# Kernel tuning notes

Hardware: AMD Instinct MI355X
Metric: run time of the kernel (lower is better)

Reference implementation:

```python
import jax, jax.numpy as jnp
import numpy as np

EPS = 1e-5

def group_norm(x, gamma, beta):
    # GroupNorm(1, C) on [N, C]: normalize over channel dim per sample
    mu = jnp.mean(x, axis=-1, keepdims=True)
    var = jnp.var(x, axis=-1, keepdims=True)
    return (x - mu) * jax.lax.rsqrt(var + EPS) * gamma + beta

def setup_inputs() -> dict:
    key = jax.random.key(0)
    ks = jax.random.split(key, 4)
    T, B, I, H = 2048, 64, 256, 512
    s1 = 1.0 / np.sqrt(H + I)
    s2 = 1.0 / np.sqrt(H)
    return {
        "input": jax.random.normal(ks[0], (T, B, I), dtype=jnp.float32),
        "W1": jax.random.uniform(ks[1], (H, H + I), jnp.float32, -s1, s1),
        "g1": jnp.ones((H,), jnp.float32), "b1": jnp.zeros((H,), jnp.float32),
        "W2": jax.random.uniform(ks[2], (H, H), jnp.float32, -s2, s2),
        "g2": jnp.ones((H,), jnp.float32), "b2": jnp.zeros((H,), jnp.float32),
        "W3": jax.random.uniform(ks[3], (3 * H, H), jnp.float32, -s2, s2),
        "g3": jnp.ones((3 * H,), jnp.float32), "b3": jnp.zeros((3 * H,), jnp.float32),
    }

def reference(input, W1, g1, b1, W2, g2, b2, W3, g3, b3):
    T, B, I = input.shape
    H = W1.shape[0]

    def step(c, x):
        z = jnp.concatenate([x, c], axis=1)              # [B, I+H]
        h = jax.nn.elu(group_norm(z @ W1.T, g1, b1))     # [B, H]
        h = jax.nn.elu(group_norm(h @ W2.T, g2, b2))     # [B, H]
        o = group_norm(h @ W3.T, g3, b3)                 # [B, 3H]
        new_hx, new_cx, forget = o[:, :H], o[:, H:2*H], o[:, 2*H:]
        f = jax.nn.sigmoid(forget) ** 2                  # sigmoid_pow(x, 2)
        retain = 1.0 - f
        hx = jax.nn.elu(new_hx)
        cx = jax.nn.elu(new_cx)
        c_new = f * cx + retain * c
        return c_new, hx

    c0 = jnp.zeros((B, H), dtype=input.dtype)
    c_final, outputs = jax.lax.scan(step, c0, input)
    return outputs, c_final[None]
```

## Files before the change

kernel.cpp:

```cpp
#include <hip/hip_runtime.h>
#include <math.h>

#define T_STEPS 2048
#define BATCH   64
#define IDIM    256
#define HDIM    512
#define K1      768
#define H3      1536
#define NGROUP  4
#define NSLICE  32
#define RPG     16
#define THREADS 512


#define OFF_A1  0
#define OFF_A2  32768
#define OFF_CB  65536
#define OFF_P3  98304
#define OFF_ST  102400

typedef __attribute__((ext_vector_type(8))) __bf16 bf16x8;
typedef __attribute__((ext_vector_type(4))) float f32x4;

__device__ __forceinline__ f32x4 MFMA(bf16x8 a, bf16x8 b, f32x4 c) {
    return __builtin_amdgcn_mfma_f32_16x16x32_bf16(a, b, c, 0, 0, 0);
}

__device__ __forceinline__ float gload(const float* p) {
    return __hip_atomic_load(p, __ATOMIC_RELAXED, __HIP_MEMORY_SCOPE_AGENT);
}
__device__ __forceinline__ void gstore(float* p, float v) {
    __hip_atomic_store(p, v, __ATOMIC_RELAXED, __HIP_MEMORY_SCOPE_AGENT);
}
__device__ __forceinline__ float2 gload2(const float* p) {
    unsigned long long v = __hip_atomic_load((const unsigned long long*)p,
                                             __ATOMIC_RELAXED, __HIP_MEMORY_SCOPE_AGENT);
    return __builtin_bit_cast(float2, v);
}
__device__ __forceinline__ void gstore2(float* p, float a, float b) {
    float2 v = {a, b};
    __hip_atomic_store((unsigned long long*)p, __builtin_bit_cast(unsigned long long, v),
                       __ATOMIC_RELAXED, __HIP_MEMORY_SCOPE_AGENT);
}
__device__ __forceinline__ int gload_i(const int* p) {
    return __hip_atomic_load(p, __ATOMIC_RELAXED, __HIP_MEMORY_SCOPE_AGENT);
}
__device__ __forceinline__ unsigned gload_u(const unsigned* p) {
    return __hip_atomic_load(p, __ATOMIC_RELAXED, __HIP_MEMORY_SCOPE_AGENT);
}
__device__ __forceinline__ void gstore_us(unsigned short* p, unsigned short v) {
    __hip_atomic_store(p, v, __ATOMIC_RELAXED, __HIP_MEMORY_SCOPE_AGENT);
}

struct bf16pair { __bf16 hi, lo; };
__device__ __forceinline__ bf16pair split2(float f) {
    bf16pair r;
    r.hi = (__bf16)f;
    r.lo = (__bf16)(f - (float)r.hi);
    return r;
}
__device__ __forceinline__ unsigned pk2(float a, float b) {
    return (unsigned)__builtin_bit_cast(unsigned short, (__bf16)a) |
           ((unsigned)__builtin_bit_cast(unsigned short, (__bf16)b) << 16);
}
__device__ __forceinline__ void st_pair(__bf16* p, __bf16 a, __bf16 b) {
    unsigned v = (unsigned)__builtin_bit_cast(unsigned short, a) |
                 ((unsigned)__builtin_bit_cast(unsigned short, b) << 16);
    *(unsigned*)p = v;
}
__device__ __forceinline__ float elu1(float v) {
    return v > 0.f ? v : (expf(v) - 1.f);
}

__device__ __forceinline__ void publish(int* stamp_s, int val) {
    __syncthreads();
    if (threadIdx.x == 0)
        __hip_atomic_store(stamp_s, val, __ATOMIC_RELAXED, __HIP_MEMORY_SCOPE_AGENT);
}
__device__ __forceinline__ void poll_release(const int* st, int target) {
    if (threadIdx.x < 64) {
        const int* p = st + (threadIdx.x & 31);
        while (true) {
            int v = gload_i(p);
            if (__all(v >= target)) break;
            __builtin_amdgcn_s_sleep(1);
        }
    }
    __syncthreads();
}

__global__ void dlstm_init(float* __restrict__ ws) {
    int idx = threadIdx.x;
    if (idx < 512) ((int*)(ws + OFF_ST))[idx] = 0;
}

__global__ __launch_bounds__(THREADS, 2) void dlstm_main(
    const float* __restrict__ x,
    const float* __restrict__ W1, const float* __restrict__ g1, const float* __restrict__ b1,
    const float* __restrict__ W2, const float* __restrict__ g2, const float* __restrict__ b2,
    const float* __restrict__ W3, const float* __restrict__ g3, const float* __restrict__ b3,
    float* __restrict__ out, float* __restrict__ ws)
{
    const int tid = threadIdx.x;
    const int bid = blockIdx.x;
    const int g = bid & 3;
    const int s = bid >> 2;
    const int r0 = g * RPG;

    const int lane = tid & 63;
    const int wv   = tid >> 6;
    const int col  = lane & 15;
    const int kq   = lane >> 4;
    const int er   = tid >> 5;
    const int l32  = tid & 31;

    float* a1 = ws + OFF_A1;
    float* a2 = ws + OFF_A2;
    unsigned short* cbu = (unsigned short*)(ws + OFF_CB);
    float* p3 = ws + OFF_P3;
    int* stb   = (int*)(ws + OFF_ST);
    int* st_a1 = stb + 0   + g * 32;
    int* st_a2 = stb + 128 + g * 32;
    int* st_p3 = stb + 256 + g * 32;
    int* st_cb = stb + 384 + g * 32;

    __shared__ __bf16 zh[16][776];
    __shared__ float comb[8][3][256];
    __shared__ float slab[16][48];
    __shared__ float stats[16][2];

    float2 g1v[8], b1v[8], g2v[8], b2v[8];
    #pragma unroll
    for (int j = 0; j < 8; ++j) {
        int k = j * 64 + l32 * 2;
        g1v[j] = *(const float2*)(g1 + k); b1v[j] = *(const float2*)(b1 + k);
        g2v[j] = *(const float2*)(g2 + k); b2v[j] = *(const float2*)(b2 + k);
    }
    float g3h = 0.f, g3c = 0.f, g3f = 0.f, b3h = 0.f, b3c = 0.f, b3f = 0.f;
    if (tid < 256) {
        int i = tid & 15; int h = 16 * s + i;
        g3h = g3[h];        g3c = g3[HDIM + h];        g3f = g3[2 * HDIM + h];
        b3h = b3[h];        b3c = b3[HDIM + h];        b3f = b3[2 * HDIM + h];
    }

    bf16x8 w1h[3], w1l[3], w2h[2], w2l[2], w3h[3][2], w3l[3][2];
    #pragma unroll
    for (int ks = 0; ks < 3; ++ks) {
        int k0 = wv * 96 + ks * 32 + kq * 8;
        const float* p = W1 + (size_t)(16 * s + col) * K1 + k0;
        #pragma unroll
        for (int e = 0; e < 8; ++e) {
            bf16pair pr = split2(p[e]);
            w1h[ks][e] = pr.hi; w1l[ks][e] = pr.lo;
        }
    }
    #pragma unroll
    for (int ks = 0; ks < 2; ++ks) {
        int k0 = wv * 64 + ks * 32 + kq * 8;
        const float* p = W2 + (size_t)(16 * s + col) * HDIM + k0;
        #pragma unroll
        for (int e = 0; e < 8; ++e) {
            bf16pair pr = split2(p[e]);
            w2h[ks][e] = pr.hi; w2l[ks][e] = pr.lo;
        }
    }
    #pragma unroll
    for (int tb = 0; tb < 3; ++tb) {
        #pragma unroll
        for (int ks = 0; ks < 2; ++ks) {
            int k0 = wv * 64 + ks * 32 + kq * 8;
            const float* p = W3 + (size_t)(tb * HDIM + 16 * s + col) * HDIM + k0;
            #pragma unroll
            for (int e = 0; e < 8; ++e) {
                bf16pair pr = split2(p[e]);
                w3h[tb][ks][e] = pr.hi; w3l[tb][ks][e] = pr.lo;
            }
        }
    }

    float creg = 0.f;

    float2 xr[4];
    unsigned xb[4];
    {
        const float* xrow = x + (size_t)(r0 + er) * IDIM;
        #pragma unroll
        for (int j = 0; j < 4; ++j) xr[j] = *(const float2*)(xrow + j * 64 + l32 * 2);
        #pragma unroll
        for (int j = 0; j < 4; ++j) xb[j] = pk2(xr[j].x, xr[j].y);
    }

    #pragma unroll 1
    for (int t = 0; t < T_STEPS; ++t) {
        unsigned* zrow = (unsigned*)&zh[er][0];
        #pragma unroll
        for (int j = 0; j < 4; ++j) zrow[j * 32 + l32] = xb[j];
        __syncthreads();
        f32x4 acc = {0.f, 0.f, 0.f, 0.f};
        #pragma unroll
        for (int ks = 0; ks < 3; ++ks) {
            int kb = wv * 96 + ks * 32;
            if (kb < IDIM) {
                bf16x8 ah = *(const bf16x8*)&zh[col][kb + kq * 8];
                acc = MFMA(ah, w1h[ks], acc);
                acc = MFMA(ah, w1l[ks], acc);
            }
        }
        if (t > 0) {
            poll_release(st_cb, t);
            const unsigned* cbrow = (const unsigned*)cbu + (size_t)(r0 + er) * (HDIM / 2);
            #pragma unroll
            for (int j = 0; j < 8; ++j)
                zrow[128 + j * 32 + l32] = gload_u(cbrow + j * 32 + l32);
        } else {
            #pragma unroll
            for (int j = 0; j < 8; ++j) zrow[128 + j * 32 + l32] = 0u;
        }
        __syncthreads();
        #pragma unroll
        for (int ks = 0; ks < 3; ++ks) {
            int kb = wv * 96 + ks * 32;
            if (kb >= IDIM) {
                bf16x8 ah = *(const bf16x8*)&zh[col][kb + kq * 8];
                acc = MFMA(ah, w1h[ks], acc);
                acc = MFMA(ah, w1l[ks], acc);
            }
        }
        #pragma unroll
        for (int i = 0; i < 4; ++i) comb[wv][0][(kq * 4 + i) * 16 + col] = acc[i];
        __syncthreads();
        if (tid < 128) {
            int r = tid >> 3, fp = tid & 7;
            int i0 = r * 16 + fp * 2;
            float v0 = 0.f, v1 = 0.f;
            #pragma unroll
            for (int w = 0; w < 8; ++w) { v0 += comb[w][0][i0]; v1 += comb[w][0][i0 + 1]; }
            gstore2(&a1[(size_t)(r0 + r) * HDIM + 16 * s + fp * 2], v0, v1);
        }
        publish(&st_a1[s], t + 1);

        poll_release(st_a1, t + 1);
        {
            size_t arow = (size_t)(r0 + er) * HDIM;
            float2 va[8]; float s1 = 0.f, s2 = 0.f;
            #pragma unroll
            for (int j = 0; j < 8; ++j) {
                va[j] = gload2(a1 + arow + j * 64 + l32 * 2);
                s1 += va[j].x + va[j].y; s2 += va[j].x * va[j].x + va[j].y * va[j].y;
            }
            s1 += __shfl_xor(s1, 1, 64); s2 += __shfl_xor(s2, 1, 64);
            s1 += __shfl_xor(s1, 2, 64); s2 += __shfl_xor(s2, 2, 64);
            s1 += __shfl_xor(s1, 4, 64); s2 += __shfl_xor(s2, 4, 64);
            s1 += __shfl_xor(s1, 8, 64); s2 += __shfl_xor(s2, 8, 64);
            s1 += __shfl_xor(s1, 16, 64); s2 += __shfl_xor(s2, 16, 64);
            float mu = s1 * (1.f / HDIM);
            float var = s2 * (1.f / HDIM) - mu * mu;
            float rs = rsqrtf(var + 1e-5f);
            #pragma unroll
            for (int j = 0; j < 8; ++j) {
                int k = j * 64 + l32 * 2;
                float v0 = elu1((va[j].x - mu) * rs * g1v[j].x + b1v[j].x);
                float v1 = elu1((va[j].y - mu) * rs * g1v[j].y + b1v[j].y);
                st_pair(&zh[er][k], (__bf16)v0, (__bf16)v1);
            }
        }
        __syncthreads();
        {
            f32x4 acc2 = {0.f, 0.f, 0.f, 0.f};
            #pragma unroll
            for (int ks = 0; ks < 2; ++ks) {
                int k0 = wv * 64 + ks * 32 + kq * 8;
                bf16x8 ah = *(const bf16x8*)&zh[col][k0];
                acc2 = MFMA(ah, w2h[ks], acc2);
                acc2 = MFMA(ah, w2l[ks], acc2);
            }
            #pragma unroll
            for (int i = 0; i < 4; ++i) comb[wv][0][(kq * 4 + i) * 16 + col] = acc2[i];
        }
        __syncthreads();
        if (tid < 128) {
            int r = tid >> 3, fp = tid & 7;
            int i0 = r * 16 + fp * 2;
            float v0 = 0.f, v1 = 0.f;
            #pragma unroll
            for (int w = 0; w < 8; ++w) { v0 += comb[w][0][i0]; v1 += comb[w][0][i0 + 1]; }
            gstore2(&a2[(size_t)(r0 + r) * HDIM + 16 * s + fp * 2], v0, v1);
        }
        publish(&st_a2[s], t + 1);

        poll_release(st_a2, t + 1);
        {
            size_t arow = (size_t)(r0 + er) * HDIM;
            float2 va[8]; float s1 = 0.f, s2 = 0.f;
            #pragma unroll
            for (int j = 0; j < 8; ++j) va[j] = gload2(a2 + arow + j * 64 + l32 * 2);
            {
                int tn = (t + 1 < T_STEPS) ? t + 1 : t;
                const float* xrow = x + ((size_t)tn * BATCH + r0 + er) * IDIM;
                #pragma unroll
                for (int j = 0; j < 4; ++j) xr[j] = *(const float2*)(xrow + j * 64 + l32 * 2);
            }
            #pragma unroll
            for (int j = 0; j < 8; ++j) {
                s1 += va[j].x + va[j].y; s2 += va[j].x * va[j].x + va[j].y * va[j].y;
            }
            s1 += __shfl_xor(s1, 1, 64); s2 += __shfl_xor(s2, 1, 64);
            s1 += __shfl_xor(s1, 2, 64); s2 += __shfl_xor(s2, 2, 64);
            s1 += __shfl_xor(s1, 4, 64); s2 += __shfl_xor(s2, 4, 64);
            s1 += __shfl_xor(s1, 8, 64); s2 += __shfl_xor(s2, 8, 64);
            s1 += __shfl_xor(s1, 16, 64); s2 += __shfl_xor(s2, 16, 64);
            float mu = s1 * (1.f / HDIM);
            float var = s2 * (1.f / HDIM) - mu * mu;
            float rs = rsqrtf(var + 1e-5f);
            #pragma unroll
            for (int j = 0; j < 8; ++j) {
                int k = j * 64 + l32 * 2;
                float v0 = elu1((va[j].x - mu) * rs * g2v[j].x + b2v[j].x);
                float v1 = elu1((va[j].y - mu) * rs * g2v[j].y + b2v[j].y);
                st_pair(&zh[er][k], (__bf16)v0, (__bf16)v1);
            }
        }
        __syncthreads();
        {
            f32x4 acc0 = {0.f,0.f,0.f,0.f}, acc1 = {0.f,0.f,0.f,0.f}, acc2 = {0.f,0.f,0.f,0.f};
            #pragma unroll
            for (int ks = 0; ks < 2; ++ks) {
                int k0 = wv * 64 + ks * 32 + kq * 8;
                bf16x8 ah = *(const bf16x8*)&zh[col][k0];
                acc0 = MFMA(ah, w3h[0][ks], acc0);
                acc0 = MFMA(ah, w3l[0][ks], acc0);
                acc1 = MFMA(ah, w3h[1][ks], acc1);
                acc1 = MFMA(ah, w3l[1][ks], acc1);
                acc2 = MFMA(ah, w3h[2][ks], acc2);
                acc2 = MFMA(ah, w3l[2][ks], acc2);
            }
            #pragma unroll
            for (int i = 0; i < 4; ++i) {
                comb[wv][0][(kq * 4 + i) * 16 + col] = acc0[i];
                comb[wv][1][(kq * 4 + i) * 16 + col] = acc1[i];
                comb[wv][2][(kq * 4 + i) * 16 + col] = acc2[i];
            }
        }
        __syncthreads();
        if (tid < 384) {
            int o = tid * 2;
            int tb = o >> 8, idx = o & 255;
            int r = idx >> 4, f0 = idx & 15;
            float v0 = 0.f, v1 = 0.f;
            #pragma unroll
            for (int w = 0; w < 8; ++w) { v0 += comb[w][tb][idx]; v1 += comb[w][tb][idx + 1]; }
            slab[r][tb * 16 + f0] = v0;
            slab[r][tb * 16 + f0 + 1] = v1;
        }
        __syncthreads();
        {
            float va_ = slab[er][l32];
            float vb_ = (l32 < 16) ? slab[er][32 + l32] : 0.f;
            float s1 = va_ + vb_;
            float s2 = va_ * va_ + vb_ * vb_;
            s1 += __shfl_xor(s1, 1, 64); s2 += __shfl_xor(s2, 1, 64);
            s1 += __shfl_xor(s1, 2, 64); s2 += __shfl_xor(s2, 2, 64);
            s1 += __shfl_xor(s1, 4, 64); s2 += __shfl_xor(s2, 4, 64);
            s1 += __shfl_xor(s1, 8, 64); s2 += __shfl_xor(s2, 8, 64);
            s1 += __shfl_xor(s1, 16, 64); s2 += __shfl_xor(s2, 16, 64);
            if (l32 == 0) gstore2(&p3[((size_t)(r0 + er) * NSLICE + s) * 2], s1, s2);
        }
        publish(&st_p3[s], t + 1);

        poll_release(st_p3, t + 1);
        {
            float2 pv = gload2(&p3[((size_t)(r0 + er) * NSLICE + l32) * 2]);
            float s1 = pv.x, s2 = pv.y;
            s1 += __shfl_xor(s1, 1, 64); s2 += __shfl_xor(s2, 1, 64);
            s1 += __shfl_xor(s1, 2, 64); s2 += __shfl_xor(s2, 2, 64);
            s1 += __shfl_xor(s1, 4, 64); s2 += __shfl_xor(s2, 4, 64);
            s1 += __shfl_xor(s1, 8, 64); s2 += __shfl_xor(s2, 8, 64);
            s1 += __shfl_xor(s1, 16, 64); s2 += __shfl_xor(s2, 16, 64);
            float mu = s1 * (1.f / H3);
            float var = s2 * (1.f / H3) - mu * mu;
            float rs = rsqrtf(var + 1e-5f);
            if (l32 == 0) { stats[er][0] = mu; stats[er][1] = rs; }
        }
        __syncthreads();
        int r_ = 0, i_ = 0;
        float mu_ = 0.f, rs_ = 0.f, cnew_ = 0.f;
        if (tid < 256) {
            r_ = tid >> 4; i_ = tid & 15;
            int h = 16 * s + i_;
            mu_ = stats[r_][0]; rs_ = stats[r_][1];
            float ocn = (slab[r_][16 + i_] - mu_) * rs_ * g3c + b3c;
            float ofn = (slab[r_][32 + i_] - mu_) * rs_ * g3f + b3f;
            float sig = 1.f / (1.f + expf(-ofn));
            float fv = sig * sig;
            cnew_ = fv * elu1(ocn) + (1.f - fv) * creg;
            creg = cnew_;
            gstore_us(&cbu[(size_t)(r_ + r0) * HDIM + h],
                      __builtin_bit_cast(unsigned short, (__bf16)cnew_));
        }
        publish(&st_cb[s], t + 1);
        if (tid < 256) {
            int h = 16 * s + i_;
            float ohn = (slab[r_][i_] - mu_) * rs_ * g3h + b3h;
            out[((size_t)t * BATCH + r0 + r_) * HDIM + h] = elu1(ohn);
            if (t == T_STEPS - 1)
                out[(size_t)T_STEPS * BATCH * HDIM + (size_t)(r0 + r_) * HDIM + h] = cnew_;
        }
        #pragma unroll
        for (int j = 0; j < 4; ++j) xb[j] = pk2(xr[j].x, xr[j].y);
    }
}

extern "C" void kernel_launch(void* const* d_in, const int* in_sizes, int n_in,
                              void* d_out, int out_size, void* d_ws, size_t ws_size,
                              hipStream_t stream) {
    const float* x  = (const float*)d_in[0];
    const float* W1 = (const float*)d_in[1];
    const float* g1 = (const float*)d_in[2];
    const float* b1 = (const float*)d_in[3];
    const float* W2 = (const float*)d_in[4];
    const float* g2 = (const float*)d_in[5];
    const float* b2 = (const float*)d_in[6];
    const float* W3 = (const float*)d_in[7];
    const float* g3 = (const float*)d_in[8];
    const float* b3 = (const float*)d_in[9];
    float* out = (float*)d_out;
    float* ws  = (float*)d_ws;

    dlstm_init<<<1, 512, 0, stream>>>(ws);
    dlstm_main<<<NGROUP * NSLICE, THREADS, 0, stream>>>(x, W1, g1, b1, W2, g2, b2, W3, g3, b3, out, ws);
}
```

Baseline: 25.78 ms.

## Prefetch next step's input MFMA during stats wait and use lightweight barriers

The input-projection half of the layer-1 MFMA for the next timestep now runs right after publishing the layer-3 partial stats, so it overlaps the cross-block wait. The cell-state half of z is zeroed once before the loop instead of every first step. Most __syncthreads calls become an inline-asm barrier that waits only on LDS counters, and the poll barrier becomes a bare s_barrier, cutting per-barrier wait overhead. The risk is correctness if the compiler-visible memory ordering around these hand-written barriers is insufficient.

```diff
diff --git a/kernel.cpp b/kernel.cpp
--- a/kernel.cpp
+++ b/kernel.cpp
@@ -26,12 +26,6 @@
     return __builtin_amdgcn_mfma_f32_16x16x32_bf16(a, b, c, 0, 0, 0);
 }
 
-__device__ __forceinline__ float gload(const float* p) {
-    return __hip_atomic_load(p, __ATOMIC_RELAXED, __HIP_MEMORY_SCOPE_AGENT);
-}
-__device__ __forceinline__ void gstore(float* p, float v) {
-    __hip_atomic_store(p, v, __ATOMIC_RELAXED, __HIP_MEMORY_SCOPE_AGENT);
-}
 __device__ __forceinline__ float2 gload2(const float* p) {
     unsigned long long v = __hip_atomic_load((const unsigned long long*)p,
                                              __ATOMIC_RELAXED, __HIP_MEMORY_SCOPE_AGENT);
@@ -70,6 +64,17 @@
 }
 __device__ __forceinline__ float elu1(float v) {
     return v > 0.f ? v : (expf(v) - 1.f);
+}
+
+__device__ __forceinline__ void lbar() {
+    __builtin_amdgcn_sched_barrier(0);
+    asm volatile("s_waitcnt lgkmcnt(0)\n\ts_barrier" ::: "memory");
+    __builtin_amdgcn_sched_barrier(0);
+}
+__device__ __forceinline__ void rbar() {
+    __builtin_amdgcn_sched_barrier(0);
+    asm volatile("s_barrier" ::: "memory");
+    __builtin_amdgcn_sched_barrier(0);
 }
 
 __device__ __forceinline__ void publish(int* stamp_s, int val) {
@@ -86,7 +91,7 @@
             __builtin_amdgcn_s_sleep(1);
         }
     }
-    __syncthreads();
+    rbar();
 }
 
 __global__ void dlstm_init(float* __restrict__ ws) {
@@ -180,43 +185,41 @@
 
     float creg = 0.f;
 
+    #pragma unroll
+    for (int k = 0; k < 8; ++k)
+        st_pair(&zh[er][256 + 2 * l32 + 64 * k], (__bf16)0.f, (__bf16)0.f);
     float2 xr[4];
-    unsigned xb[4];
     {
         const float* xrow = x + (size_t)(r0 + er) * IDIM;
         #pragma unroll
         for (int j = 0; j < 4; ++j) xr[j] = *(const float2*)(xrow + j * 64 + l32 * 2);
-        #pragma unroll
-        for (int j = 0; j < 4; ++j) xb[j] = pk2(xr[j].x, xr[j].y);
+        unsigned* zrow = (unsigned*)&zh[er][0];
+        #pragma unroll
+        for (int j = 0; j < 4; ++j) zrow[j * 32 + l32] = pk2(xr[j].x, xr[j].y);
+    }
+    __syncthreads();
+    f32x4 acc = {0.f, 0.f, 0.f, 0.f};
+    #pragma unroll
+    for (int ks = 0; ks < 3; ++ks) {
+        int kb = wv * 96 + ks * 32;
+        if (kb < IDIM) {
+            bf16x8 ah = *(const bf16x8*)&zh[col][kb + kq * 8];
+            acc = MFMA(ah, w1h[ks], acc);
+            acc = MFMA(ah, w1l[ks], acc);
+        }
     }
 
     #pragma unroll 1
     for (int t = 0; t < T_STEPS; ++t) {
         unsigned* zrow = (unsigned*)&zh[er][0];
-        #pragma unroll
-        for (int j = 0; j < 4; ++j) zrow[j * 32 + l32] = xb[j];
-        __syncthreads();
-        f32x4 acc = {0.f, 0.f, 0.f, 0.f};
-        #pragma unroll
-        for (int ks = 0; ks < 3; ++ks) {
-            int kb = wv * 96 + ks * 32;
-            if (kb < IDIM) {
-                bf16x8 ah = *(const bf16x8*)&zh[col][kb + kq * 8];
-                acc = MFMA(ah, w1h[ks], acc);
-                acc = MFMA(ah, w1l[ks], acc);
-            }
-        }
         if (t > 0) {
             poll_release(st_cb, t);
             const unsigned* cbrow = (const unsigned*)cbu + (size_t)(r0 + er) * (HDIM / 2);
             #pragma unroll
             for (int j = 0; j < 8; ++j)
                 zrow[128 + j * 32 + l32] = gload_u(cbrow + j * 32 + l32);
-        } else {
-            #pragma unroll
-            for (int j = 0; j < 8; ++j) zrow[128 + j * 32 + l32] = 0u;
-        }
-        __syncthreads();
+        }
+        lbar();
         #pragma unroll
         for (int ks = 0; ks < 3; ++ks) {
             int kb = wv * 96 + ks * 32;
@@ -228,7 +231,7 @@
         }
         #pragma unroll
         for (int i = 0; i < 4; ++i) comb[wv][0][(kq * 4 + i) * 16 + col] = acc[i];
-        __syncthreads();
+        lbar();
         if (tid < 128) {
             int r = tid >> 3, fp = tid & 7;
             int i0 = r * 16 + fp * 2;
@@ -264,7 +267,7 @@
                 st_pair(&zh[er][k], (__bf16)v0, (__bf16)v1);
             }
         }
-        __syncthreads();
+        lbar();
         {
             f32x4 acc2 = {0.f, 0.f, 0.f, 0.f};
             #pragma unroll
@@ -277,7 +280,7 @@
             #pragma unroll
             for (int i = 0; i < 4; ++i) comb[wv][0][(kq * 4 + i) * 16 + col] = acc2[i];
         }
-        __syncthreads();
+        lbar();
         if (tid < 128) {
             int r = tid >> 3, fp = tid & 7;
             int i0 = r * 16 + fp * 2;
@@ -320,7 +323,7 @@
                 st_pair(&zh[er][k], (__bf16)v0, (__bf16)v1);
             }
         }
-        __syncthreads();
+        lbar();
         {
             f32x4 acc0 = {0.f,0.f,0.f,0.f}, acc1 = {0.f,0.f,0.f,0.f}, acc2 = {0.f,0.f,0.f,0.f};
             #pragma unroll
@@ -341,7 +344,7 @@
                 comb[wv][2][(kq * 4 + i) * 16 + col] = acc2[i];
             }
         }
-        __syncthreads();
+        lbar();
         if (tid < 384) {
             int o = tid * 2;
             int tb = o >> 8, idx = o & 255;
@@ -352,7 +355,11 @@
             slab[r][tb * 16 + f0] = v0;
             slab[r][tb * 16 + f0 + 1] = v1;
         }
-        __syncthreads();
+        {
+            #pragma unroll
+            for (int j = 0; j < 4; ++j) zrow[j * 32 + l32] = pk2(xr[j].x, xr[j].y);
+        }
+        lbar();
         {
             float va_ = slab[er][l32];
             float vb_ = (l32 < 16) ? slab[er][32 + l32] : 0.f;
@@ -366,6 +373,17 @@
             if (l32 == 0) gstore2(&p3[((size_t)(r0 + er) * NSLICE + s) * 2], s1, s2);
         }
         publish(&st_p3[s], t + 1);
+
+        acc[0] = 0.f; acc[1] = 0.f; acc[2] = 0.f; acc[3] = 0.f;
+        #pragma unroll
+        for (int ks = 0; ks < 3; ++ks) {
+            int kb = wv * 96 + ks * 32;
+            if (kb < IDIM) {
+                bf16x8 ah = *(const bf16x8*)&zh[col][kb + kq * 8];
+                acc = MFMA(ah, w1h[ks], acc);
+                acc = MFMA(ah, w1l[ks], acc);
+            }
+        }
 
         poll_release(st_p3, t + 1);
         {
@@ -381,7 +399,7 @@
             float rs = rsqrtf(var + 1e-5f);
             if (l32 == 0) { stats[er][0] = mu; stats[er][1] = rs; }
         }
-        __syncthreads();
+        lbar();
         int r_ = 0, i_ = 0;
         float mu_ = 0.f, rs_ = 0.f, cnew_ = 0.f;
         if (tid < 256) {
@@ -405,8 +423,6 @@
             if (t == T_STEPS - 1)
                 out[(size_t)T_STEPS * BATCH * HDIM + (size_t)(r0 + r_) * HDIM + h] = cnew_;
         }
-        #pragma unroll
-        for (int j = 0; j < 4; ++j) xb[j] = pk2(xr[j].x, xr[j].y);
     }
 }
 
```

Measured after the change: 26.71 ms. +3.6%, slower.

## Replace block-wide publish barriers with per-wave atomic counter publication

Applied to the files above, without the earlier changes.

Removes the __syncthreads in each publish step. Each wave now waits on its own outstanding memory ops, bumps a shared-memory counter, and the last wave to arrive writes the global stamp. Global stores become atomic exchanges, which return only after completion so vmcnt covers them. The c-state stores are packed into 32-bit pairs through a shuffle instead of 16-bit stores. This shortens the critical path between producer and consumer blocks in the persistent cross-block pipeline, at the risk of subtle memory-ordering bugs.

```diff
diff --git a/kernel.cpp b/kernel.cpp
--- a/kernel.cpp
+++ b/kernel.cpp
@@ -26,30 +26,28 @@
     return __builtin_amdgcn_mfma_f32_16x16x32_bf16(a, b, c, 0, 0, 0);
 }
 
-__device__ __forceinline__ float gload(const float* p) {
-    return __hip_atomic_load(p, __ATOMIC_RELAXED, __HIP_MEMORY_SCOPE_AGENT);
-}
-__device__ __forceinline__ void gstore(float* p, float v) {
-    __hip_atomic_store(p, v, __ATOMIC_RELAXED, __HIP_MEMORY_SCOPE_AGENT);
-}
 __device__ __forceinline__ float2 gload2(const float* p) {
     unsigned long long v = __hip_atomic_load((const unsigned long long*)p,
                                              __ATOMIC_RELAXED, __HIP_MEMORY_SCOPE_AGENT);
     return __builtin_bit_cast(float2, v);
 }
-__device__ __forceinline__ void gstore2(float* p, float a, float b) {
-    float2 v = {a, b};
-    __hip_atomic_store((unsigned long long*)p, __builtin_bit_cast(unsigned long long, v),
-                       __ATOMIC_RELAXED, __HIP_MEMORY_SCOPE_AGENT);
-}
 __device__ __forceinline__ int gload_i(const int* p) {
     return __hip_atomic_load(p, __ATOMIC_RELAXED, __HIP_MEMORY_SCOPE_AGENT);
 }
 __device__ __forceinline__ unsigned gload_u(const unsigned* p) {
     return __hip_atomic_load(p, __ATOMIC_RELAXED, __HIP_MEMORY_SCOPE_AGENT);
 }
-__device__ __forceinline__ void gstore_us(unsigned short* p, unsigned short v) {
-    __hip_atomic_store(p, v, __ATOMIC_RELAXED, __HIP_MEMORY_SCOPE_AGENT);
+__device__ __forceinline__ void gswap2(float* p, float a, float b) {
+    float2 v = {a, b};
+    (void)__hip_atomic_exchange((unsigned long long*)p,
+                                __builtin_bit_cast(unsigned long long, v),
+                                __ATOMIC_RELAXED, __HIP_MEMORY_SCOPE_AGENT);
+}
+__device__ __forceinline__ void gswap_u(unsigned* p, unsigned v) {
+    (void)__hip_atomic_exchange(p, v, __ATOMIC_RELAXED, __HIP_MEMORY_SCOPE_AGENT);
+}
+__device__ __forceinline__ void gswap_i(int* p, int v) {
+    (void)__hip_atomic_exchange(p, v, __ATOMIC_RELAXED, __HIP_MEMORY_SCOPE_AGENT);
 }
 
 struct bf16pair { __bf16 hi, lo; };
@@ -72,10 +70,13 @@
     return v > 0.f ? v : (expf(v) - 1.f);
 }
 
-__device__ __forceinline__ void publish(int* stamp_s, int val) {
-    __syncthreads();
-    if (threadIdx.x == 0)
-        __hip_atomic_store(stamp_s, val, __ATOMIC_RELAXED, __HIP_MEMORY_SCOPE_AGENT);
+__device__ __forceinline__ void wave_pub(int* lds_ctr, int finish_old, int* stamp, int val) {
+    asm volatile("s_waitcnt vmcnt(0)" ::: "memory");
+    if ((threadIdx.x & 63) == 0) {
+        int old = __hip_atomic_fetch_add(lds_ctr, 1, __ATOMIC_RELAXED,
+                                         __HIP_MEMORY_SCOPE_WORKGROUP);
+        if (old == finish_old) gswap_i(stamp, val);
+    }
 }
 __device__ __forceinline__ void poll_release(const int* st, int target) {
     if (threadIdx.x < 64) {
@@ -116,7 +117,7 @@
 
     float* a1 = ws + OFF_A1;
     float* a2 = ws + OFF_A2;
-    unsigned short* cbu = (unsigned short*)(ws + OFF_CB);
+    unsigned* cb32 = (unsigned*)(ws + OFF_CB);
     float* p3 = ws + OFF_P3;
     int* stb   = (int*)(ws + OFF_ST);
     int* st_a1 = stb + 0   + g * 32;
@@ -128,6 +129,9 @@
     __shared__ float comb[8][3][256];
     __shared__ float slab[16][48];
     __shared__ float stats[16][2];
+    __shared__ int syncc[4];
+
+    if (tid < 4) syncc[tid] = 0;
 
     float2 g1v[8], b1v[8], g2v[8], b2v[8];
     #pragma unroll
@@ -208,7 +212,7 @@
         }
         if (t > 0) {
             poll_release(st_cb, t);
-            const unsigned* cbrow = (const unsigned*)cbu + (size_t)(r0 + er) * (HDIM / 2);
+            const unsigned* cbrow = cb32 + (size_t)(r0 + er) * (HDIM / 2);
             #pragma unroll
             for (int j = 0; j < 8; ++j)
                 zrow[128 + j * 32 + l32] = gload_u(cbrow + j * 32 + l32);
@@ -235,9 +239,9 @@
             float v0 = 0.f, v1 = 0.f;
             #pragma unroll
             for (int w = 0; w < 8; ++w) { v0 += comb[w][0][i0]; v1 += comb[w][0][i0 + 1]; }
-            gstore2(&a1[(size_t)(r0 + r) * HDIM + 16 * s + fp * 2], v0, v1);
-        }
-        publish(&st_a1[s], t + 1);
+            gswap2(&a1[(size_t)(r0 + r) * HDIM + 16 * s + fp * 2], v0, v1);
+            wave_pub(&syncc[0], 2 * t + 1, &st_a1[s], t + 1);
+        }
 
         poll_release(st_a1, t + 1);
         {
@@ -284,9 +288,9 @@
             float v0 = 0.f, v1 = 0.f;
             #pragma unroll
             for (int w = 0; w < 8; ++w) { v0 += comb[w][0][i0]; v1 += comb[w][0][i0 + 1]; }
-            gstore2(&a2[(size_t)(r0 + r) * HDIM + 16 * s + fp * 2], v0, v1);
-        }
-        publish(&st_a2[s], t + 1);
+            gswap2(&a2[(size_t)(r0 + r) * HDIM + 16 * s + fp * 2], v0, v1);
+            wave_pub(&syncc[1], 2 * t + 1, &st_a2[s], t + 1);
+        }
 
         poll_release(st_a2, t + 1);
         {
@@ -363,9 +367,9 @@
             s1 += __shfl_xor(s1, 4, 64); s2 += __shfl_xor(s2, 4, 64);
             s1 += __shfl_xor(s1, 8, 64); s2 += __shfl_xor(s2, 8, 64);
             s1 += __shfl_xor(s1, 16, 64); s2 += __shfl_xor(s2, 16, 64);
-            if (l32 == 0) gstore2(&p3[((size_t)(r0 + er) * NSLICE + s) * 2], s1, s2);
-        }
-        publish(&st_p3[s], t + 1);
+            if (l32 == 0) gswap2(&p3[((size_t)(r0 + er) * NSLICE + s) * 2], s1, s2);
+        }
+        wave_pub(&syncc[2], 8 * t + 7, &st_p3[s], t + 1);
 
         poll_release(st_p3, t + 1);
         {
@@ -386,7 +390,6 @@
         float mu_ = 0.f, rs_ = 0.f, cnew_ = 0.f;
         if (tid < 256) {
             r_ = tid >> 4; i_ = tid & 15;
-            int h = 16 * s + i_;
             mu_ = stats[r_][0]; rs_ = stats[r_][1];
             float ocn = (slab[r_][16 + i_] - mu_) * rs_ * g3c + b3c;
             float ofn = (slab[r_][32 + i_] - mu_) * rs_ * g3f + b3f;
@@ -394,11 +397,11 @@
             float fv = sig * sig;
             cnew_ = fv * elu1(ocn) + (1.f - fv) * creg;
             creg = cnew_;
-            gstore_us(&cbu[(size_t)(r_ + r0) * HDIM + h],
-                      __builtin_bit_cast(unsigned short, (__bf16)cnew_));
-        }
-        publish(&st_cb[s], t + 1);
-        if (tid < 256) {
+            float cnx = __shfl_down(cnew_, 1, 64);
+            if ((i_ & 1) == 0)
+                gswap_u(cb32 + (size_t)(r_ + r0) * (HDIM / 2) + 8 * s + (i_ >> 1),
+                        pk2(cnew_, cnx));
+            wave_pub(&syncc[3], 4 * t + 3, &st_cb[s], t + 1);
             int h = 16 * s + i_;
             float ohn = (slab[r_][i_] - mu_) * rs_ * g3h + b3h;
             out[((size_t)t * BATCH + r0 + r_) * HDIM + h] = elu1(ohn);
```

Result: slower. 29.97 ms (+16.2%).
